# Kernel tuning notes

Hardware: AMD Instinct MI355X
Metric: run time of the kernel (lower is better)

Reference implementation:

```python
import jax, jax.numpy as jnp
import numpy as np

BS, H, W, A, NC, G = 2048, 14, 14, 5, 2, 30
SIZE = 1 + NC + 4  # conf, classes, x, y, w, h
OBJ_SCALE, NOOBJ_SCALE, CLASS_SCALE, COORD_SCALE = 5.0, 0.5, 1.0, 1.0


def setup_inputs() -> dict:
    key = jax.random.key(0)
    pred = jax.random.normal(key, (BS, A * SIZE, H, W), dtype=jnp.float32) * 0.5
    # Structured label: G ground-truth boxes per image at distinct cells.
    rng = np.random.default_rng(0)
    lab = np.zeros((BS, 7, H, W), np.float32)
    perm = np.argsort(rng.random((BS, H * W)), axis=1)[:, :G]  # distinct cells
    r, c = perm // W, perm % W
    b = np.arange(BS)[:, None]
    lab[b, 0, r, c] = 1.0
    cls = rng.integers(0, 2, (BS, G)).astype(np.float32)
    lab[b, 1, r, c] = cls
    lab[b, 2, r, c] = 1.0 - cls
    lab[b, 3, r, c] = rng.uniform(0.1, 0.9, (BS, G))  # tx in-cell offset
    lab[b, 4, r, c] = rng.uniform(0.1, 0.9, (BS, G))  # ty
    lab[b, 5, r, c] = rng.uniform(0.05, 0.4, (BS, G))  # tw (normalized)
    lab[b, 6, r, c] = rng.uniform(0.05, 0.4, (BS, G))  # th
    anchors = np.array([[42.0, 44.0], [91.0, 104.0], [162.0, 220.0],
                        [299.0, 170.0], [396.0, 359.0]], np.float32)
    return {"pred": pred, "label": jnp.asarray(lab),
            "anchors": jnp.asarray(anchors), "seen": 6400}


def _yolo_v2_loss(pred, label, anchors, seen):
    f32 = jnp.float32
    anchor_bias = anchors / (512.0 / 14.0) / jnp.array([W, H], f32)  # [A,2], grid-normalized
    # [BS,H,W,A,SIZE]
    pred_r = pred.transpose(0, 2, 3, 1).reshape(BS, H, W, A, SIZE)
    sxy = jax.nn.sigmoid(pred_r[..., 1 + NC:3 + NC])               # sigmoid(x,y)
    ids = jnp.stack(jnp.meshgrid(jnp.arange(W, dtype=f32),
                                 jnp.arange(H, dtype=f32)), -1)[:, :, None, :]  # [H,W,1,2]=(c,r)
    coords = (sxy + ids) / jnp.array([W, H], f32)                  # normalized centers
    wh = jnp.exp(pred_r[..., 3 + NC:5 + NC]) * anchor_bias         # normalized w,h
    boxes = jnp.concatenate([coords, wh], -1)                      # [BS,H,W,A,4]
    aw, ah = anchor_bias[:, 0], anchor_bias[:, 1]

    def per_image(pred_b, sxy_b, boxes_b, label_b):
        obj = label_b[0].reshape(-1)
        vals, flat = jax.lax.top_k(obj, G)
        valid = vals > 0                                           # [G]
        r = flat // W
        c = flat % W
        tx, ty = label_b[3, r, c], label_b[4, r, c]
        tw = jnp.where(valid, label_b[5, r, c], 1.0)
        th = jnp.where(valid, label_b[6, r, c], 1.0)
        # gt boxes are built from detached .data in the torch code -> stop_gradient
        gx = jax.lax.stop_gradient((tx + c.astype(f32)) / W)
        gy = jax.lax.stop_gradient((ty + r.astype(f32)) / H)
        tw = jax.lax.stop_gradient(tw)
        th = jax.lax.stop_gradient(th)
        # pairwise IoU pred boxes [H,W,A] vs gt [G] -> [H,W,A,G]
        x1, y1 = boxes_b[..., 0:1], boxes_b[..., 1:2]
        w1, h1 = boxes_b[..., 2:3], boxes_b[..., 3:4]
        xi1 = jnp.maximum(x1 - 0.5 * w1, gx - 0.5 * tw)
        yi1 = jnp.maximum(y1 - 0.5 * h1, gy - 0.5 * th)
        xi2 = jnp.minimum(x1 + 0.5 * w1, gx + 0.5 * tw)
        yi2 = jnp.minimum(y1 + 0.5 * h1, gy + 0.5 * th)
        inter = jnp.maximum(xi2 - xi1, 0.0) * jnp.maximum(yi2 - yi1, 0.0)
        union = w1 * h1 + tw * th - inter
        iou = jnp.maximum(inter / union, 0.0)
        iou = jnp.where(valid, iou, 0.0)
        noobj = (iou.max(-1) <= 0.6).astype(f32) * (NOOBJ_SCALE * pred_b[..., 0])
        if seen < 12800:
            prior = 0.01 * jnp.concatenate([sxy_b - 0.5,
                                            pred_b[..., 3 + NC:5 + NC]], -1)
        else:
            prior = jnp.zeros((H, W, A, 4), f32)
        coord_obj = jnp.concatenate([prior, noobj[..., None]], -1)  # [H,W,A,5]
        # best anchor per gt (IoU of (0,0,tw,th) vs (0,0,aw,ah))
        ia = jnp.minimum(tw[:, None], aw) * jnp.minimum(th[:, None], ah)
        aid = jnp.argmax(ia / (tw[:, None] * th[:, None] + aw * ah - ia), axis=1)
        wi = (gx * W).astype(jnp.int32)
        fx = gx * W - wi.astype(f32)
        hj = (gy * H).astype(jnp.int32)
        fy = gy * H - hj.astype(f32)
        twh = jnp.log(jnp.stack([tw, th], 1) / anchor_bias[aid])    # [G,2]
        truth_coords = jnp.concatenate([fx[:, None], fy[:, None], twh], 1)
        p_sel = pred_b[hj, wi, aid]                                 # [G,SIZE]
        pc = jnp.concatenate([sxy_b[hj, wi, aid], p_sel[:, 3 + NC:5 + NC]], 1)
        wgt = COORD_SCALE * (2.0 - fx * fy)                         # detached in torch
        closs = wgt[:, None] * (pc - truth_coords)                  # [G,4]
        iou_sel = iou[hj, wi, aid, jnp.arange(G)]                   # [G]
        objl = OBJ_SCALE * (p_sel[:, 0] - iou_sel)
        tco = jnp.concatenate([closs, objl[:, None]], 1) * valid[:, None].astype(f32)
        cvec = jnp.stack([label_b[1, hj, wi], label_b[2, hj, wi]], 1)
        cls_l = CLASS_SCALE * (p_sel[:, 1:1 + NC] - cvec)
        loss_cls = jnp.sum((cls_l ** 2) * valid[:, None].astype(f32))
        m = jnp.zeros((H, W, A), f32).at[hj, wi, aid].add(valid.astype(f32))
        ta = jnp.zeros((H, W, A, 5), f32).at[hj, wi, aid].add(tco)
        m4 = m[..., None]
        comb = m4 * ta + (1.0 - m4) * coord_obj
        il = loss_cls + jnp.sum(comb ** 2)
        return jnp.where(jnp.any(valid), il, 0.0)

    losses = jax.vmap(per_image)(pred_r, sxy, boxes, label)
    return jnp.reshape(jnp.sum(losses) / BS, (1,))


def reference(pred, label, anchors, seen):
    return _yolo_v2_loss(pred, label, anchors, seen)
```

## Files before the change

kernel.cpp:

```cpp
#include <hip/hip_runtime.h>
#include <math.h>

#define BS 2048
#define H_ 14
#define W_ 14
#define A_ 5
#define G_ 30
#define HW_ 196
#define NTHREADS 256
#define LABN (7 * HW_)
#define LAB4 (LABN / 4)
#define NQ 245

typedef _Float16 h2 __attribute__((ext_vector_type(2)));

__device__ __forceinline__ float fast_rcp(float x) { return __builtin_amdgcn_rcpf(x); }
__device__ __forceinline__ h2 h2max(h2 a, h2 b) { return __builtin_elementwise_max(a, b); }
__device__ __forceinline__ h2 h2min(h2 a, h2 b) { return __builtin_elementwise_min(a, b); }
__device__ __forceinline__ h2 h2bc(float x) { h2 r; r[0] = (_Float16)x; r[1] = r[0]; return r; }

__global__ __launch_bounds__(NTHREADS) void yolo_main(
    const float* __restrict__ pred,
    const float* __restrict__ label,
    const float* __restrict__ anchors,
    float* __restrict__ partial)
{
    __shared__ float  s_lab[LABN];
    __shared__ uint4  s_geo[16];
    __shared__ unsigned int s_nth[16];
    __shared__ float4 s_ebox[32];
    __shared__ float4 s_tgt[32];
    __shared__ float4 s_aux[32];
    __shared__ float  s_aw[A_], s_ah[A_];
    __shared__ char   s_map[992] __attribute__((aligned(16)));
    __shared__ int    s_flat[G_];
    __shared__ int    s_wcnt[NTHREADS / 64];
    __shared__ float  s_red[NTHREADS / 64];

    const int b    = blockIdx.x;
    const int tid  = threadIdx.x;
    const int lane = tid & 63;
    const int wv   = tid >> 6;
    const float* lb = label + (size_t)b * LABN;
    const float* pb = pred  + (size_t)b * (A_ * 7 * HW_);

    float objv = (tid < HW_) ? lb[tid] : 0.0f;

    {
        const float4* l4 = (const float4*)lb;
        float4* s4 = (float4*)s_lab;
        for (int i = tid; i < LAB4; i += NTHREADS) s4[i] = l4[i];
    }
    if (tid < 62) ((int4*)s_map)[tid] = make_int4(-1, -1, -1, -1);
    if (tid < A_) {
        const float div1 = 512.0f / 14.0f;
        s_aw[tid] = anchors[2 * tid]     / div1;
        s_ah[tid] = anchors[2 * tid + 1] / div1;
    }

    unsigned long long bm = __ballot(objv > 0.0f);
    if (lane == 0) s_wcnt[wv] = __popcll(bm);
    __syncthreads();
    if (objv > 0.0f) {
        int rank = __popcll(bm & ((1ULL << lane) - 1ULL));
        for (int w2 = 0; w2 < wv; ++w2) rank += s_wcnt[w2];
        s_flat[rank] = tid;
    }
    __syncthreads();

    if (tid < G_) {
        int flat = s_flat[tid];
        int r = flat / W_, c = flat - r * W_;
        float tx = s_lab[3 * HW_ + flat];
        float ty = s_lab[4 * HW_ + flat];
        float tw = s_lab[5 * HW_ + flat];
        float th = s_lab[6 * HW_ + flat];
        float gxg = tx + (float)c;
        float gyg = ty + (float)r;
        int   wi = (int)gxg;
        int   hj = (int)gyg;
        float fx = gxg - (float)wi;
        float fy = gyg - (float)hj;
        float best = -1.0f; int aid = 0;
        for (int aa = 0; aa < A_; ++aa) {
            float awn = s_aw[aa] / 14.0f;
            float ahn = s_ah[aa] / 14.0f;
            float ia = fminf(tw, awn) * fminf(th, ahn);
            float m  = ia / (tw * th + awn * ahn - ia);
            if (m > best) { best = m; aid = aa; }
        }
        float awn = s_aw[aid] / 14.0f, ahn = s_ah[aid] / 14.0f;
        float twg = tw * 14.0f, thg = th * 14.0f;
        float x1 = gxg - 0.5f * twg, y1 = gyg - 0.5f * thg;
        float x2 = gxg + 0.5f * twg, y2 = gyg + 0.5f * thg;
        float areag = twg * thg;
        s_ebox[tid] = make_float4(x1, y1, x2, y2);
        s_tgt[tid]  = make_float4(fx, fy, __logf(tw / awn), __logf(th / ahn));
        s_aux[tid]  = make_float4(2.0f - fx * fy,
                                  s_lab[1 * HW_ + hj * W_ + wi],
                                  s_lab[2 * HW_ + hj * W_ + wi],
                                  areag);
        s_map[(hj * W_ + wi) * A_ + aid] = (char)tid;

        _Float16* gp = (_Float16*)s_geo;
        _Float16* np = (_Float16*)s_nth;
        int p = tid >> 1, e = tid & 1;
        gp[8 * p + 0 + e] = (_Float16)x1;
        gp[8 * p + 2 + e] = (_Float16)y1;
        gp[8 * p + 4 + e] = (_Float16)x2;
        gp[8 * p + 6 + e] = (_Float16)y2;
        np[2 * p + e]     = (_Float16)(-0.375f * areag);
        if (tid < 2) {
            int g2 = 30 + tid, p2 = g2 >> 1, e2 = g2 & 1;
            gp[8 * p2 + 0 + e2] = (_Float16)x1;
            gp[8 * p2 + 2 + e2] = (_Float16)y1;
            gp[8 * p2 + 4 + e2] = (_Float16)x2;
            gp[8 * p2 + 6 + e2] = (_Float16)y2;
            np[2 * p2 + e2]     = (_Float16)(-0.375f * areag);
        }
    }
    __syncthreads();

    float lsum = 0.0f;
    if (tid < NQ) {
        int a   = tid / 49;
        int qq  = tid - a * 49;
        int hw0 = 4 * qq;
        const float4* p4 = (const float4*)(pb + a * 7 * HW_);
        float4 P0 = p4[0 * 49 + qq];
        float4 P3 = p4[3 * 49 + qq];
        float4 P4 = p4[4 * 49 + qq];
        float4 P5 = p4[5 * 49 + qq];
        float4 P6 = p4[6 * 49 + qq];
        float p0v[4] = {P0.x, P0.y, P0.z, P0.w};
        float p3v[4] = {P3.x, P3.y, P3.z, P3.w};
        float p4v[4] = {P4.x, P4.y, P4.z, P4.w};
        float p5v[4] = {P5.x, P5.y, P5.z, P5.w};
        float p6v[4] = {P6.x, P6.y, P6.z, P6.w};

        float aw = s_aw[a], ah = s_ah[a];
        float sxv[4], syv[4], bwv[4], bhv[4];
        h2 xlo2[4], xhi2[4], ylo2[4], yhi2[4], acc2[4];
        const h2 hz = h2bc(0.0f);
        #pragma unroll
        for (int j = 0; j < 4; ++j) {
            int hw = hw0 + j;
            int h  = hw / W_;
            int w  = hw - h * W_;
            float sx = fast_rcp(1.0f + __expf(-p3v[j]));
            float sy = fast_rcp(1.0f + __expf(-p4v[j]));
            float bw = __expf(p5v[j]) * aw;
            float bh = __expf(p6v[j]) * ah;
            float x1 = sx + (float)w;
            float y1 = sy + (float)h;
            sxv[j] = sx;  syv[j] = sy;  bwv[j] = bw;  bhv[j] = bh;
            xlo2[j] = h2bc(x1 - 0.5f * bw);
            xhi2[j] = h2bc(x1 + 0.5f * bw);
            ylo2[j] = h2bc(y1 - 0.5f * bh);
            yhi2[j] = h2bc(y1 + 0.5f * bh);
            acc2[j] = h2bc(-30000.0f);
        }

        #pragma unroll 4
        for (int p = 0; p < 16; ++p) {
            uint4 Gq = s_geo[p];
            h2 X1 = __builtin_bit_cast(h2, Gq.x);
            h2 Y1 = __builtin_bit_cast(h2, Gq.y);
            h2 X2 = __builtin_bit_cast(h2, Gq.z);
            h2 Y2 = __builtin_bit_cast(h2, Gq.w);
            h2 NT = __builtin_bit_cast(h2, s_nth[p]);
            #pragma unroll
            for (int j = 0; j < 4; ++j) {
                h2 xi1 = h2max(xlo2[j], X1);
                h2 yi1 = h2max(ylo2[j], Y1);
                h2 xi2 = h2min(xhi2[j], X2);
                h2 yi2 = h2min(yhi2[j], Y2);
                h2 dx = h2max(xi2 - xi1, hz);
                h2 dy = h2max(yi2 - yi1, hz);
                acc2[j] = h2max(acc2[j], dx * dy + NT);
            }
        }

        float4 R1 = p4[1 * 49 + qq];
        float4 R2 = p4[2 * 49 + qq];
        float p1v[4] = {R1.x, R1.y, R1.z, R1.w};
        float p2v[4] = {R2.x, R2.y, R2.z, R2.w};

        #pragma unroll
        for (int j = 0; j < 4; ++j) {
            int hw = hw0 + j;
            int h  = hw / W_;
            int w  = hw - h * W_;
            int g_at = (int)s_map[hw * A_ + a];
            float area1 = bwv[j] * bhv[j];
            if (g_at >= 0) {
                float4 tg = s_tgt[g_at];
                float4 u  = s_aux[g_at];
                float4 bx = s_ebox[g_at];
                float x1 = sxv[j] + (float)w, y1 = syv[j] + (float)h;
                float xlo = x1 - 0.5f * bwv[j], xhi = x1 + 0.5f * bwv[j];
                float ylo = y1 - 0.5f * bhv[j], yhi = y1 + 0.5f * bhv[j];
                float xi1 = fmaxf(xlo, bx.x);
                float yi1 = fmaxf(ylo, bx.y);
                float xi2 = fminf(xhi, bx.z);
                float yi2 = fminf(yhi, bx.w);
                float inter = fmaxf(xi2 - xi1, 0.0f) * fmaxf(yi2 - yi1, 0.0f);
                float uni   = area1 + u.w - inter;
                float iou   = fmaxf(inter * fast_rcp(uni), 0.0f);
                float wg = u.x;
                float d0 = wg * (sxv[j] - tg.x);
                float d1 = wg * (syv[j] - tg.y);
                float d2 = wg * (p5v[j] - tg.z);
                float d3 = wg * (p6v[j] - tg.w);
                float ob = 5.0f * (p0v[j] - iou);
                float c1 = p1v[j] - u.y;
                float c2 = p2v[j] - u.z;
                lsum += d0*d0 + d1*d1 + d2*d2 + d3*d3 + ob*ob + c1*c1 + c2*c2;
            } else {
                float accf = fmaxf((float)acc2[j][0], (float)acc2[j][1]);
                float pr0 = 0.01f * (sxv[j] - 0.5f);
                float pr1 = 0.01f * (syv[j] - 0.5f);
                float pr2 = 0.01f * p5v[j];
                float pr3 = 0.01f * p6v[j];
                float no  = (accf <= 0.375f * area1) ? 0.5f * p0v[j] : 0.0f;
                lsum += pr0*pr0 + pr1*pr1 + pr2*pr2 + pr3*pr3 + no*no;
            }
        }
    }

    #pragma unroll
    for (int off = 32; off > 0; off >>= 1)
        lsum += __shfl_down(lsum, off, 64);
    if (lane == 0) s_red[wv] = lsum;
    __syncthreads();
    if (tid == 0) {
        float tot = 0.0f;
        #pragma unroll
        for (int i = 0; i < NTHREADS / 64; ++i) tot += s_red[i];
        partial[b] = tot;
    }
}

__global__ __launch_bounds__(NTHREADS) void yolo_reduce(
    const float* __restrict__ partial, float* __restrict__ out)
{
    __shared__ float s_red[NTHREADS / 64];
    const int tid = threadIdx.x, lane = tid & 63, wv = tid >> 6;
    float s = 0.0f;
    for (int i = tid; i < BS; i += NTHREADS) s += partial[i];
    #pragma unroll
    for (int off = 32; off > 0; off >>= 1)
        s += __shfl_down(s, off, 64);
    if (lane == 0) s_red[wv] = s;
    __syncthreads();
    if (tid == 0) {
        float tot = 0.0f;
        #pragma unroll
        for (int i = 0; i < NTHREADS / 64; ++i) tot += s_red[i];
        out[0] = tot * (1.0f / (float)BS);
    }
}

extern "C" void kernel_launch(void* const* d_in, const int* in_sizes, int n_in,
                              void* d_out, int out_size, void* d_ws, size_t ws_size,
                              hipStream_t stream) {
    const float* pred    = (const float*)d_in[0];
    const float* label   = (const float*)d_in[1];
    const float* anchors = (const float*)d_in[2];
    float* out     = (float*)d_out;
    float* partial = (float*)d_ws;

    yolo_main<<<dim3(BS), dim3(NTHREADS), 0, stream>>>(pred, label, anchors, partial);
    yolo_reduce<<<dim3(1), dim3(NTHREADS), 0, stream>>>(partial, out);
}
```

Before: 111.5 us.

## Compute no-object loss for all cells, correct matched GT cells separately

The per-cell branch on a shared anchor map is replaced by a branch-free no-object loss computed for every cell. A separate pass over the 30 ground-truth entries recomputes each matched cell's contributions and subtracts the no-object term it would have added. Prediction loads are issued before the label staging and barriers so they overlap. GT extraction is moved to a single wavefront, which removes the map initialisation, one barrier and the class-channel loads for unmatched cells. The cost is redundant IoU work for matched cells and a subtraction that can add rounding error.

```diff
diff --git a/kernel.cpp b/kernel.cpp
--- a/kernel.cpp
+++ b/kernel.cpp
@@ -28,13 +28,12 @@
     __shared__ float  s_lab[LABN];
     __shared__ uint4  s_geo[16];
     __shared__ unsigned int s_nth[16];
-    __shared__ float4 s_ebox[32];
-    __shared__ float4 s_tgt[32];
-    __shared__ float4 s_aux[32];
+    __shared__ float4 s_ebox[G_];
+    __shared__ float4 s_tgt[G_];
+    __shared__ float4 s_aux[G_];
     __shared__ float  s_aw[A_], s_ah[A_];
-    __shared__ char   s_map[992] __attribute__((aligned(16)));
     __shared__ int    s_flat[G_];
-    __shared__ int    s_wcnt[NTHREADS / 64];
+    __shared__ int    s_gaid[G_];
     __shared__ float  s_red[NTHREADS / 64];
 
     const int b    = blockIdx.x;
@@ -44,94 +43,94 @@
     const float* lb = label + (size_t)b * LABN;
     const float* pb = pred  + (size_t)b * (A_ * 7 * HW_);
 
-    float objv = (tid < HW_) ? lb[tid] : 0.0f;
+    const bool act = tid < NQ;
+    const int  qt  = act ? tid : NQ - 1;
+    const int  a   = qt / 49;
+    const int  qq  = qt - a * 49;
+    const int  hw0 = 4 * qq;
+    const float4* p4 = (const float4*)(pb + a * 7 * HW_);
+    float4 P0 = p4[0 * 49 + qq];
+    float4 P3 = p4[3 * 49 + qq];
+    float4 P4 = p4[4 * 49 + qq];
+    float4 P5 = p4[5 * 49 + qq];
+    float4 P6 = p4[6 * 49 + qq];
 
     {
         const float4* l4 = (const float4*)lb;
         float4* s4 = (float4*)s_lab;
-        for (int i = tid; i < LAB4; i += NTHREADS) s4[i] = l4[i];
-    }
-    if (tid < 62) ((int4*)s_map)[tid] = make_int4(-1, -1, -1, -1);
+        s4[tid] = l4[tid];
+        if (tid < LAB4 - NTHREADS) s4[NTHREADS + tid] = l4[NTHREADS + tid];
+    }
     if (tid < A_) {
         const float div1 = 512.0f / 14.0f;
         s_aw[tid] = anchors[2 * tid]     / div1;
         s_ah[tid] = anchors[2 * tid + 1] / div1;
     }
-
-    unsigned long long bm = __ballot(objv > 0.0f);
-    if (lane == 0) s_wcnt[wv] = __popcll(bm);
     __syncthreads();
-    if (objv > 0.0f) {
-        int rank = __popcll(bm & ((1ULL << lane) - 1ULL));
-        for (int w2 = 0; w2 < wv; ++w2) rank += s_wcnt[w2];
-        s_flat[rank] = tid;
+
+    if (wv == 0) {
+        int base = 0;
+        #pragma unroll
+        for (int k = 0; k < 4; ++k) {
+            int idx = k * 64 + lane;
+            float v = (idx < HW_) ? s_lab[idx] : 0.0f;
+            unsigned long long m = __ballot(v > 0.0f);
+            if (v > 0.0f) s_flat[base + __popcll(m & ((1ULL << lane) - 1ULL))] = idx;
+            base += __popcll(m);
+        }
+        if (lane < G_) {
+            int flat = s_flat[lane];
+            int r = flat / W_, c = flat - r * W_;
+            float tx = s_lab[3 * HW_ + flat];
+            float ty = s_lab[4 * HW_ + flat];
+            float tw = s_lab[5 * HW_ + flat];
+            float th = s_lab[6 * HW_ + flat];
+            float gxg = tx + (float)c;
+            float gyg = ty + (float)r;
+            float fx = gxg - (float)c;
+            float fy = gyg - (float)r;
+            float best = -1.0f; int aid = 0;
+            for (int aa = 0; aa < A_; ++aa) {
+                float awn = s_aw[aa] / 14.0f;
+                float ahn = s_ah[aa] / 14.0f;
+                float ia = fminf(tw, awn) * fminf(th, ahn);
+                float m  = ia / (tw * th + awn * ahn - ia);
+                if (m > best) { best = m; aid = aa; }
+            }
+            float awn = s_aw[aid] / 14.0f, ahn = s_ah[aid] / 14.0f;
+            float twg = tw * 14.0f, thg = th * 14.0f;
+            float x1 = gxg - 0.5f * twg, y1 = gyg - 0.5f * thg;
+            float x2 = gxg + 0.5f * twg, y2 = gyg + 0.5f * thg;
+            float areag = twg * thg;
+            s_ebox[lane] = make_float4(x1, y1, x2, y2);
+            s_tgt[lane]  = make_float4(fx, fy, __logf(tw / awn), __logf(th / ahn));
+            s_aux[lane]  = make_float4(2.0f - fx * fy,
+                                       s_lab[1 * HW_ + flat],
+                                       s_lab[2 * HW_ + flat],
+                                       areag);
+            s_gaid[lane] = aid;
+            _Float16* gp = (_Float16*)s_geo;
+            _Float16* np = (_Float16*)s_nth;
+            int p = lane >> 1, e = lane & 1;
+            gp[8 * p + 0 + e] = (_Float16)x1;
+            gp[8 * p + 2 + e] = (_Float16)y1;
+            gp[8 * p + 4 + e] = (_Float16)x2;
+            gp[8 * p + 6 + e] = (_Float16)y2;
+            np[2 * p + e]     = (_Float16)(-0.375f * areag);
+            if (lane < 2) {
+                int g2 = 30 + lane, p2 = g2 >> 1, e2 = g2 & 1;
+                gp[8 * p2 + 0 + e2] = (_Float16)x1;
+                gp[8 * p2 + 2 + e2] = (_Float16)y1;
+                gp[8 * p2 + 4 + e2] = (_Float16)x2;
+                gp[8 * p2 + 6 + e2] = (_Float16)y2;
+                np[2 * p2 + e2]     = (_Float16)(-0.375f * areag);
+            }
+        }
     }
     __syncthreads();
 
-    if (tid < G_) {
-        int flat = s_flat[tid];
-        int r = flat / W_, c = flat - r * W_;
-        float tx = s_lab[3 * HW_ + flat];
-        float ty = s_lab[4 * HW_ + flat];
-        float tw = s_lab[5 * HW_ + flat];
-        float th = s_lab[6 * HW_ + flat];
-        float gxg = tx + (float)c;
-        float gyg = ty + (float)r;
-        int   wi = (int)gxg;
-        int   hj = (int)gyg;
-        float fx = gxg - (float)wi;
-        float fy = gyg - (float)hj;
-        float best = -1.0f; int aid = 0;
-        for (int aa = 0; aa < A_; ++aa) {
-            float awn = s_aw[aa] / 14.0f;
-            float ahn = s_ah[aa] / 14.0f;
-            float ia = fminf(tw, awn) * fminf(th, ahn);
-            float m  = ia / (tw * th + awn * ahn - ia);
-            if (m > best) { best = m; aid = aa; }
-        }
-        float awn = s_aw[aid] / 14.0f, ahn = s_ah[aid] / 14.0f;
-        float twg = tw * 14.0f, thg = th * 14.0f;
-        float x1 = gxg - 0.5f * twg, y1 = gyg - 0.5f * thg;
-        float x2 = gxg + 0.5f * twg, y2 = gyg + 0.5f * thg;
-        float areag = twg * thg;
-        s_ebox[tid] = make_float4(x1, y1, x2, y2);
-        s_tgt[tid]  = make_float4(fx, fy, __logf(tw / awn), __logf(th / ahn));
-        s_aux[tid]  = make_float4(2.0f - fx * fy,
-                                  s_lab[1 * HW_ + hj * W_ + wi],
-                                  s_lab[2 * HW_ + hj * W_ + wi],
-                                  areag);
-        s_map[(hj * W_ + wi) * A_ + aid] = (char)tid;
-
-        _Float16* gp = (_Float16*)s_geo;
-        _Float16* np = (_Float16*)s_nth;
-        int p = tid >> 1, e = tid & 1;
-        gp[8 * p + 0 + e] = (_Float16)x1;
-        gp[8 * p + 2 + e] = (_Float16)y1;
-        gp[8 * p + 4 + e] = (_Float16)x2;
-        gp[8 * p + 6 + e] = (_Float16)y2;
-        np[2 * p + e]     = (_Float16)(-0.375f * areag);
-        if (tid < 2) {
-            int g2 = 30 + tid, p2 = g2 >> 1, e2 = g2 & 1;
-            gp[8 * p2 + 0 + e2] = (_Float16)x1;
-            gp[8 * p2 + 2 + e2] = (_Float16)y1;
-            gp[8 * p2 + 4 + e2] = (_Float16)x2;
-            gp[8 * p2 + 6 + e2] = (_Float16)y2;
-            np[2 * p2 + e2]     = (_Float16)(-0.375f * areag);
-        }
-    }
-    __syncthreads();
-
     float lsum = 0.0f;
-    if (tid < NQ) {
-        int a   = tid / 49;
-        int qq  = tid - a * 49;
-        int hw0 = 4 * qq;
-        const float4* p4 = (const float4*)(pb + a * 7 * HW_);
-        float4 P0 = p4[0 * 49 + qq];
-        float4 P3 = p4[3 * 49 + qq];
-        float4 P4 = p4[4 * 49 + qq];
-        float4 P5 = p4[5 * 49 + qq];
-        float4 P6 = p4[6 * 49 + qq];
+    if (act) {
         float p0v[4] = {P0.x, P0.y, P0.z, P0.w};
         float p3v[4] = {P3.x, P3.y, P3.z, P3.w};
         float p4v[4] = {P4.x, P4.y, P4.z, P4.w};
@@ -139,9 +138,10 @@
         float p6v[4] = {P6.x, P6.y, P6.z, P6.w};
 
         float aw = s_aw[a], ah = s_ah[a];
-        float sxv[4], syv[4], bwv[4], bhv[4];
+        float thr0[4];
         h2 xlo2[4], xhi2[4], ylo2[4], yhi2[4], acc2[4];
         const h2 hz = h2bc(0.0f);
+        float hacc = 0.0f;
         #pragma unroll
         for (int j = 0; j < 4; ++j) {
             int hw = hw0 + j;
@@ -153,12 +153,14 @@
             float bh = __expf(p6v[j]) * ah;
             float x1 = sx + (float)w;
             float y1 = sy + (float)h;
-            sxv[j] = sx;  syv[j] = sy;  bwv[j] = bw;  bhv[j] = bh;
             xlo2[j] = h2bc(x1 - 0.5f * bw);
             xhi2[j] = h2bc(x1 + 0.5f * bw);
             ylo2[j] = h2bc(y1 - 0.5f * bh);
             yhi2[j] = h2bc(y1 + 0.5f * bh);
+            thr0[j] = 0.375f * (bw * bh);
             acc2[j] = h2bc(-30000.0f);
+            float dsx = sx - 0.5f, dsy = sy - 0.5f;
+            hacc += dsx * dsx + dsy * dsy + p5v[j] * p5v[j] + p6v[j] * p6v[j];
         }
 
         #pragma unroll 4
@@ -181,51 +183,78 @@
             }
         }
 
-        float4 R1 = p4[1 * 49 + qq];
-        float4 R2 = p4[2 * 49 + qq];
-        float p1v[4] = {R1.x, R1.y, R1.z, R1.w};
-        float p2v[4] = {R2.x, R2.y, R2.z, R2.w};
-
+        float nacc = 0.0f;
         #pragma unroll
         for (int j = 0; j < 4; ++j) {
-            int hw = hw0 + j;
-            int h  = hw / W_;
-            int w  = hw - h * W_;
-            int g_at = (int)s_map[hw * A_ + a];
-            float area1 = bwv[j] * bhv[j];
-            if (g_at >= 0) {
-                float4 tg = s_tgt[g_at];
-                float4 u  = s_aux[g_at];
-                float4 bx = s_ebox[g_at];
-                float x1 = sxv[j] + (float)w, y1 = syv[j] + (float)h;
-                float xlo = x1 - 0.5f * bwv[j], xhi = x1 + 0.5f * bwv[j];
-                float ylo = y1 - 0.5f * bhv[j], yhi = y1 + 0.5f * bhv[j];
-                float xi1 = fmaxf(xlo, bx.x);
-                float yi1 = fmaxf(ylo, bx.y);
-                float xi2 = fminf(xhi, bx.z);
-                float yi2 = fminf(yhi, bx.w);
-                float inter = fmaxf(xi2 - xi1, 0.0f) * fmaxf(yi2 - yi1, 0.0f);
-                float uni   = area1 + u.w - inter;
-                float iou   = fmaxf(inter * fast_rcp(uni), 0.0f);
-                float wg = u.x;
-                float d0 = wg * (sxv[j] - tg.x);
-                float d1 = wg * (syv[j] - tg.y);
-                float d2 = wg * (p5v[j] - tg.z);
-                float d3 = wg * (p6v[j] - tg.w);
-                float ob = 5.0f * (p0v[j] - iou);
-                float c1 = p1v[j] - u.y;
-                float c2 = p2v[j] - u.z;
-                lsum += d0*d0 + d1*d1 + d2*d2 + d3*d3 + ob*ob + c1*c1 + c2*c2;
-            } else {
-                float accf = fmaxf((float)acc2[j][0], (float)acc2[j][1]);
-                float pr0 = 0.01f * (sxv[j] - 0.5f);
-                float pr1 = 0.01f * (syv[j] - 0.5f);
-                float pr2 = 0.01f * p5v[j];
-                float pr3 = 0.01f * p6v[j];
-                float no  = (accf <= 0.375f * area1) ? 0.5f * p0v[j] : 0.0f;
-                lsum += pr0*pr0 + pr1*pr1 + pr2*pr2 + pr3*pr3 + no*no;
-            }
-        }
+            float accf = fmaxf((float)acc2[j][0], (float)acc2[j][1]);
+            nacc += (accf <= thr0[j]) ? p0v[j] * p0v[j] : 0.0f;
+        }
+        lsum = 1e-4f * hacc + 0.25f * nacc;
+    }
+
+    if (wv == 0 && lane < G_) {
+        int flat = s_flat[lane];
+        int aid  = s_gaid[lane];
+        const float* pc = pb + aid * 7 * HW_ + flat;
+        float q0 = pc[0];
+        float q1 = pc[1 * HW_];
+        float q2 = pc[2 * HW_];
+        float q3 = pc[3 * HW_];
+        float q4 = pc[4 * HW_];
+        float q5 = pc[5 * HW_];
+        float q6 = pc[6 * HW_];
+        int r = flat / W_, c = flat - r * W_;
+        float aw2 = s_aw[aid], ah2 = s_ah[aid];
+        float sx = fast_rcp(1.0f + __expf(-q3));
+        float sy = fast_rcp(1.0f + __expf(-q4));
+        float bw = __expf(q5) * aw2;
+        float bh = __expf(q6) * ah2;
+        float x1 = sx + (float)c, y1 = sy + (float)r;
+        float xlo = x1 - 0.5f * bw, xhi = x1 + 0.5f * bw;
+        float ylo = y1 - 0.5f * bh, yhi = y1 + 0.5f * bh;
+        float area1 = bw * bh, thr0 = 0.375f * area1;
+        h2 xl = h2bc(xlo), xh = h2bc(xhi), yl = h2bc(ylo), yh = h2bc(yhi);
+        h2 acc = h2bc(-30000.0f);
+        const h2 hz = h2bc(0.0f);
+        #pragma unroll 4
+        for (int p = 0; p < 16; ++p) {
+            uint4 Gq = s_geo[p];
+            h2 X1 = __builtin_bit_cast(h2, Gq.x);
+            h2 Y1 = __builtin_bit_cast(h2, Gq.y);
+            h2 X2 = __builtin_bit_cast(h2, Gq.z);
+            h2 Y2 = __builtin_bit_cast(h2, Gq.w);
+            h2 NT = __builtin_bit_cast(h2, s_nth[p]);
+            h2 xi1 = h2max(xl, X1);
+            h2 yi1 = h2max(yl, Y1);
+            h2 xi2 = h2min(xh, X2);
+            h2 yi2 = h2min(yh, Y2);
+            h2 dx = h2max(xi2 - xi1, hz);
+            h2 dy = h2max(yi2 - yi1, hz);
+            acc = h2max(acc, dx * dy + NT);
+        }
+        float accf = fmaxf((float)acc[0], (float)acc[1]);
+        float dsx = sx - 0.5f, dsy = sy - 0.5f;
+        float Wc = 1e-4f * (dsx * dsx + dsy * dsy + q5 * q5 + q6 * q6)
+                 + ((accf <= thr0) ? 0.25f * q0 * q0 : 0.0f);
+        float4 tg = s_tgt[lane];
+        float4 u  = s_aux[lane];
+        float4 bx = s_ebox[lane];
+        float xi1 = fmaxf(xlo, bx.x);
+        float yi1 = fmaxf(ylo, bx.y);
+        float xi2 = fminf(xhi, bx.z);
+        float yi2 = fminf(yhi, bx.w);
+        float inter = fmaxf(xi2 - xi1, 0.0f) * fmaxf(yi2 - yi1, 0.0f);
+        float uni   = area1 + u.w - inter;
+        float iou   = fmaxf(inter * fast_rcp(uni), 0.0f);
+        float wg = u.x;
+        float d0 = wg * (sx - tg.x);
+        float d1 = wg * (sy - tg.y);
+        float d2 = wg * (q5 - tg.z);
+        float d3 = wg * (q6 - tg.w);
+        float ob = 5.0f * (q0 - iou);
+        float c1 = q1 - u.y;
+        float c2 = q2 - u.z;
+        lsum += (d0*d0 + d1*d1 + d2*d2 + d3*d3 + ob*ob + c1*c1 + c2*c2) - Wc;
     }
 
     #pragma unroll
```

Measured after the change: 113.5 us. Within noise of the previous version (+1.8%).
